# Performance work log

Hardware: AMD Instinct MI355X
Metric: run time of the kernel (lower is better)

## Reference

```python
import jax, jax.numpy as jnp
import numpy as np

D_MODEL = 1024
NUM_HEADS = 2
NUM_FEATURES = 256
DEPTH = D_MODEL // 2  # faithful to source: depth = d_model // 2
B, L = 4, 4096


def _orthogonal_gaussian(key, m, d):
    # Faithful port of orthogonal_gaussian: stacked QR blocks, scaled.
    num_squares = m // d
    remainder = m - d * num_squares
    keys = jax.random.split(key, num_squares + 1)
    blocks = []
    for i in range(num_squares):
        q, _ = jnp.linalg.qr(jax.random.normal(keys[i], (d, d)))
        blocks.append(q.T)
    if remainder:
        q, _ = jnp.linalg.qr(jax.random.normal(keys[-1], (d, d)))
        blocks.append(q.T[:remainder])
    mat = jnp.vstack(blocks)
    return mat / jnp.sqrt(jnp.float32(num_squares) + remainder / d)


def setup_inputs() -> dict:
    key = jax.random.key(0)
    ks = jax.random.split(key, 16)
    s = 0.02
    inp = {
        'query': jax.random.normal(ks[0], (B, L, D_MODEL), jnp.float32),
        'key':   jax.random.normal(ks[1], (B, L, D_MODEL), jnp.float32),
        'value': jax.random.normal(ks[2], (B, L, D_MODEL), jnp.float32),
        'mask':  jnp.zeros((B, 1, 1, L), jnp.float32),
        'Wq': jax.random.normal(ks[3], (D_MODEL, D_MODEL), jnp.float32) * s,
        'bq': jnp.zeros((D_MODEL,), jnp.float32),
        'Wk': jax.random.normal(ks[4], (D_MODEL, D_MODEL), jnp.float32) * s,
        'bk': jnp.zeros((D_MODEL,), jnp.float32),
        'Wv': jax.random.normal(ks[5], (D_MODEL, D_MODEL), jnp.float32) * s,
        'bv': jnp.zeros((D_MODEL,), jnp.float32),
        'Wo': jax.random.normal(ks[6], (D_MODEL, D_MODEL), jnp.float32) * s,
        'bo': jnp.zeros((D_MODEL,), jnp.float32),
        'random_feats': _orthogonal_gaussian(ks[7], NUM_FEATURES, DEPTH),
    }
    return inp


def _softmax_kernel(data, is_query, proj, eps=1e-6):
    # data: [B, L, H, D]; proj: [M, D]
    d = data.shape[-1]
    data = data * (1.0 / jnp.sqrt(jnp.sqrt(jnp.float32(d))))
    ratio = 1.0 / jnp.sqrt(jnp.float32(proj.shape[0]))
    data_dash = jnp.einsum('blhd,md->blhm', data, proj)  # [B,L,H,M]
    diag = jnp.sum(data * data, axis=-1, keepdims=True) * 0.5  # [B,L,H,1]
    if is_query:
        mx = jnp.max(data_dash, axis=-1, keepdims=True)
    else:
        # last_dims_t + attention_dims_t = (3, 1)
        mx = jnp.max(data_dash, axis=(3, 1), keepdims=True)
    return ratio * (jnp.exp(data_dash - diag - mx) + eps)


def _attn_hat(q, k, v, proj):
    # q,k,v: [B, H, Lh, D]  (Lh = 2L/num_heads from split_heads quirk)
    l = q.shape[0]  # faithful: tf.shape(query)[0] == batch
    q = jnp.transpose(q, (0, 2, 1, 3))  # [B, Lh, H, D]
    k = jnp.transpose(k, (0, 2, 1, 3))
    q_prime = _softmax_kernel(q, True, proj)   # [B, Lh, H, M]
    k_prime = _softmax_kernel(k, False, proj)
    v = jnp.transpose(v, (0, 2, 1, 3))         # [B, Lh, H, D]
    # Faithful einsums: axis0 labeled 'l' (=batch), axis1 labeled 'b' (=seq)
    av = jnp.einsum('lbhm,lbhd->bhmd', k_prime, v)
    av = jnp.einsum('lbhm,bhmd->lbhd', q_prime, av)
    norm = jnp.einsum('lbhm,l->bhm', k_prime, jnp.ones((l,), jnp.float32))
    norm = jnp.einsum('lbhm,bhm->lbh', q_prime, norm)
    av = jnp.transpose(av, (1, 0, 2, 3))       # [Lh, B, H, D]
    norm = jnp.transpose(norm, (1, 0, 2))[..., None]
    return av / norm


def reference(query, key, value, mask, Wq, bq, Wk, bk, Wv, bv, Wo, bo, random_feats):
    bsz = query.shape[0]
    q = query @ Wq + bq
    k = key @ Wk + bk
    v = value @ Wv + bv

    def split_heads(x):
        x = x.reshape(bsz, -1, NUM_HEADS, DEPTH)
        return jnp.transpose(x, (0, 2, 1, 3))

    q, k, v = split_heads(q), split_heads(k), split_heads(v)
    attn = _attn_hat(q, k, v, random_feats)        # [Lh, B, H, D]
    attn = jnp.transpose(attn, (0, 2, 1, 3))       # [Lh, H, B, D]
    concat = attn.reshape(bsz, -1, D_MODEL)
    return concat @ Wo + bo
```

## Files before the change

### kernel.cpp

```cpp
#include <hip/hip_runtime.h>
#include <cstdint>
#include <cstddef>

typedef unsigned short u16;
typedef __bf16 bf16x8 __attribute__((ext_vector_type(8)));
typedef float   f32x4 __attribute__((ext_vector_type(4)));

#define D_MODEL 1024
#define NF      256
#define DEPTH   512
#define SEQ     4096
#define ROWS    16384
#define HROWS   32768

#define QK_SCALE      0.21022410381342864f
#define HALF_SCALE2   0.022097086912079608f

__device__ __forceinline__ u16 f2bf(float f) {
  union { float f; uint32_t u; } x; x.f = f;
  uint32_t r = x.u + 0x7FFFu + ((x.u >> 16) & 1u);
  return (u16)(r >> 16);
}
__device__ __forceinline__ float bf2f(u16 u) {
  union { uint32_t u; float f; } x; x.u = ((uint32_t)u) << 16;
  return x.f;
}

__device__ __forceinline__ void gload16(const u16* g, u16* l) {
  __builtin_amdgcn_global_load_lds((const __attribute__((address_space(1))) void*)g,
                                   (__attribute__((address_space(3))) void*)l,
                                   16, 0, 0);
}


__global__ void cvt_kernel(const float4* __restrict__ s0, const float4* __restrict__ s1,
                           const float4* __restrict__ s2, ushort4* __restrict__ d0,
                           ushort4* __restrict__ d1, ushort4* __restrict__ d2) {
  const float4* s = (blockIdx.y == 0) ? s0 : (blockIdx.y == 1) ? s1 : s2;
  ushort4* d      = (blockIdx.y == 0) ? d0 : (blockIdx.y == 1) ? d1 : d2;
  int t = blockIdx.x * 512 + threadIdx.x;
  float4 a = s[t];
  float4 b = s[t + 256];
  d[t]       = make_ushort4(f2bf(a.x), f2bf(a.y), f2bf(a.z), f2bf(a.w));
  d[t + 256] = make_ushort4(f2bf(b.x), f2bf(b.y), f2bf(b.z), f2bf(b.w));
}

__global__ void transpose4_kernel(const float* __restrict__ w0, const float* __restrict__ w1,
                                  const float* __restrict__ w2, const float* __restrict__ w3,
                                  u16* __restrict__ o0, u16* __restrict__ o1,
                                  u16* __restrict__ o2, u16* __restrict__ o3) {
  __shared__ float tile[32][33];
  int z = blockIdx.z;
  const float* src = (z == 0) ? w0 : (z == 1) ? w1 : (z == 2) ? w2 : w3;
  u16* dst         = (z == 0) ? o0 : (z == 1) ? o1 : (z == 2) ? o2 : o3;
  int bx = blockIdx.x * 32, by = blockIdx.y * 32;
  int tx = threadIdx.x, ty = threadIdx.y;
#pragma unroll
  for (int r = ty; r < 32; r += 8) tile[r][tx] = src[(size_t)(by + r) * D_MODEL + bx + tx];
  __syncthreads();
#pragma unroll
  for (int r = ty; r < 32; r += 8)
    dst[(size_t)(bx + r) * D_MODEL + by + tx] = f2bf(tile[tx][r]);
}

__global__ void projcvt_kernel(const float4* __restrict__ p, ushort4* __restrict__ o) {
  int i = blockIdx.x * 256 + threadIdx.x;
  float4 a = p[i];
  o[i] = make_ushort4(f2bf(a.x * QK_SCALE), f2bf(a.y * QK_SCALE),
                      f2bf(a.z * QK_SCALE), f2bf(a.w * QK_SCALE));
}

template <bool BF16OUT>
__global__ __launch_bounds__(256) void gemm_bt_kernel(
    const u16* __restrict__ A, const u16* __restrict__ B, void* __restrict__ Cv,
    const float* __restrict__ bias, int K, int N) {
  __shared__ __align__(16) u16 As[128 * 32];
  __shared__ __align__(16) u16 Bs[128 * 32];
  const int tid  = threadIdx.x;
  const int lane = tid & 63;
  const int wave = tid >> 6;
  const int wm = wave >> 1, wn = wave & 1;
  const int quad = lane >> 4, l15 = lane & 15;
  const int bm = blockIdx.y, bn = blockIdx.x;
  const u16* Ab = A + (size_t)bm * 128 * K;
  const u16* Bb = B + (size_t)bn * 128 * K;

  const int srow = lane >> 2;
  const int scol = (lane & 3) * 8;
  const u16* Ag0 = Ab + (size_t)(wave * 32 + srow) * K + scol;
  const u16* Ag1 = Ag0 + (size_t)16 * K;
  const u16* Bg0 = Bb + (size_t)(wave * 32 + srow) * K + scol;
  const u16* Bg1 = Bg0 + (size_t)16 * K;
  u16* lA0 = As + wave * 1024;
  u16* lA1 = lA0 + 512;
  u16* lB0 = Bs + wave * 1024;
  u16* lB1 = lB0 + 512;

  f32x4 acc[4][4] = {};

  for (int k0 = 0; k0 < K; k0 += 32) {
    __syncthreads();
    gload16(Ag0 + k0, lA0);
    gload16(Ag1 + k0, lA1);
    gload16(Bg0 + k0, lB0);
    gload16(Bg1 + k0, lB1);
    __syncthreads();
    bf16x8 af[4], bfr[4];
#pragma unroll
    for (int mt = 0; mt < 4; mt++)
      af[mt] = *(const bf16x8*)&As[(wm * 64 + mt * 16 + l15) * 32 + quad * 8];
#pragma unroll
    for (int nt = 0; nt < 4; nt++)
      bfr[nt] = *(const bf16x8*)&Bs[(wn * 64 + nt * 16 + l15) * 32 + quad * 8];
#pragma unroll
    for (int mt = 0; mt < 4; mt++)
#pragma unroll
      for (int nt = 0; nt < 4; nt++)
        acc[mt][nt] = __builtin_amdgcn_mfma_f32_16x16x32_bf16(af[mt], bfr[nt], acc[mt][nt], 0, 0, 0);
  }

  const int rbase = bm * 128 + wm * 64 + quad * 4;
  const int cbase = bn * 128 + wn * 64 + l15;
#pragma unroll
  for (int nt = 0; nt < 4; nt++) {
    int col = cbase + nt * 16;
    float bvad = bias ? bias[col] : 0.0f;
#pragma unroll
    for (int mt = 0; mt < 4; mt++) {
#pragma unroll
      for (int r = 0; r < 4; r++) {
        int row = rbase + mt * 16 + r;
        float v = acc[mt][nt][r] + bvad;
        if (BF16OUT) ((u16*)Cv)[(size_t)row * N + col] = f2bf(v);
        else         ((float*)Cv)[(size_t)row * N + col] = v;
      }
    }
  }
}

__global__ void diag_kernel(const u16* __restrict__ Qb, const u16* __restrict__ Kb,
                            float* __restrict__ dq, float* __restrict__ dk) {
  const int wave = threadIdx.x >> 6, lane = threadIdx.x & 63;
  int row = blockIdx.x * 4 + wave;
  const u16* src; float* dst; int r;
  if (row < HROWS) { src = Qb; dst = dq; r = row; }
  else             { src = Kb; dst = dk; r = row - HROWS; }
  const ushort4* p = (const ushort4*)(src + (size_t)r * DEPTH);
  ushort4 u0 = p[lane * 2], u1 = p[lane * 2 + 1];
  float s = 0.f, f;
  f = bf2f(u0.x); s += f * f; f = bf2f(u0.y); s += f * f;
  f = bf2f(u0.z); s += f * f; f = bf2f(u0.w); s += f * f;
  f = bf2f(u1.x); s += f * f; f = bf2f(u1.y); s += f * f;
  f = bf2f(u1.z); s += f * f; f = bf2f(u1.w); s += f * f;
#pragma unroll
  for (int o = 32; o; o >>= 1) s += __shfl_xor(s, o);
  if (lane == 0) dst[r] = s * HALF_SCALE2;
}

__global__ void maxk_part_kernel(const float* __restrict__ kd, float* __restrict__ partials) {
  int g = blockIdx.x >> 6;
  int sb = blockIdx.x & 63;
  int b = g >> 1, h = g & 1;
  int tid = threadIdx.x;
  float mx = -3.4e38f;
  for (int j = 0; j < 64; j++) {
    int s = sb * 64 + j;
    int row = b * 8192 + s * 2 + h;
    mx = fmaxf(mx, kd[(size_t)row * NF + tid]);
  }
#pragma unroll
  for (int o = 32; o; o >>= 1) mx = fmaxf(mx, __shfl_xor(mx, o));
  __shared__ float wmax[4];
  if ((tid & 63) == 0) wmax[tid >> 6] = mx;
  __syncthreads();
  if (tid == 0)
    partials[blockIdx.x] = fmaxf(fmaxf(wmax[0], wmax[1]), fmaxf(wmax[2], wmax[3]));
}

__global__ void maxk_final_kernel(const float* __restrict__ partials, float* __restrict__ mxk) {
  float v = partials[blockIdx.x * 64 + threadIdx.x];
#pragma unroll
  for (int o = 32; o; o >>= 1) v = fmaxf(v, __shfl_xor(v, o));
  if (threadIdx.x == 0) mxk[blockIdx.x] = v;
}

__global__ __launch_bounds__(256) void attn_kernel(
    const float* __restrict__ qd, const float* __restrict__ kd,
    const float* __restrict__ diagq, const float* __restrict__ diagk,
    const float* __restrict__ mxk, const u16* __restrict__ Vb,
    u16* __restrict__ concat) {
  int s = blockIdx.x >> 1, h = blockIdx.x & 1;
  int t = threadIdx.x;
  int wave = t >> 6, lane = t & 63;
  __shared__ float qp[4][256], kp[4][256];
  __shared__ float As[4][4];
  __shared__ float wred[4][4];
  __shared__ float mqs[4];

  float qv[4], kv[4];
  int rows[4];
#pragma unroll
  for (int b = 0; b < 4; b++) {
    int r = b * 8192 + s * 2 + h;
    rows[b] = r;
    qv[b] = qd[(size_t)r * NF + t];
    kv[b] = kd[(size_t)r * NF + t];
  }
#pragma unroll
  for (int b = 0; b < 4; b++) {
    float v = qv[b];
#pragma unroll
    for (int o = 32; o; o >>= 1) v = fmaxf(v, __shfl_xor(v, o));
    if (lane == 0) wred[wave][b] = v;
  }
  __syncthreads();
  if (t < 4) mqs[t] = fmaxf(fmaxf(wred[0][t], wred[1][t]), fmaxf(wred[2][t], wred[3][t]));
  __syncthreads();
#pragma unroll
  for (int b = 0; b < 4; b++) {
    qp[b][t] = __expf(qv[b] - diagq[rows[b]] - mqs[b]) + 1e-6f;
    kp[b][t] = __expf(kv[b] - diagk[rows[b]] - mxk[b * 2 + h]) + 1e-6f;
  }
  __syncthreads();
  {
    int i = wave;
    float p0 = 0, p1 = 0, p2 = 0, p3 = 0;
    for (int m = lane; m < 256; m += 64) {
      float q = qp[i][m];
      p0 += q * kp[0][m]; p1 += q * kp[1][m];
      p2 += q * kp[2][m]; p3 += q * kp[3][m];
    }
#pragma unroll
    for (int o = 32; o; o >>= 1) {
      p0 += __shfl_xor(p0, o); p1 += __shfl_xor(p1, o);
      p2 += __shfl_xor(p2, o); p3 += __shfl_xor(p3, o);
    }
    if (lane == 0) { As[i][0] = p0; As[i][1] = p1; As[i][2] = p2; As[i][3] = p3; }
  }
  __syncthreads();
  float a00 = As[0][0], a01 = As[0][1], a02 = As[0][2], a03 = As[0][3];
  float a10 = As[1][0], a11 = As[1][1], a12 = As[1][2], a13 = As[1][3];
  float a20 = As[2][0], a21 = As[2][1], a22 = As[2][2], a23 = As[2][3];
  float a30 = As[3][0], a31 = As[3][1], a32 = As[3][2], a33 = As[3][3];
  float n0 = 1.f / (a00 + a01 + a02 + a03);
  float n1 = 1.f / (a10 + a11 + a12 + a13);
  float n2 = 1.f / (a20 + a21 + a22 + a23);
  float n3 = 1.f / (a30 + a31 + a32 + a33);
  size_t obase = (size_t)s * 4096 + (size_t)h * 2048;
#pragma unroll
  for (int dp = 0; dp < 2; dp++) {
    int d = t + dp * 256;
    float v0 = bf2f(Vb[((size_t)(0 * SEQ + s)) * D_MODEL + h * DEPTH + d]);
    float v1 = bf2f(Vb[((size_t)(1 * SEQ + s)) * D_MODEL + h * DEPTH + d]);
    float v2 = bf2f(Vb[((size_t)(2 * SEQ + s)) * D_MODEL + h * DEPTH + d]);
    float v3 = bf2f(Vb[((size_t)(3 * SEQ + s)) * D_MODEL + h * DEPTH + d]);
    concat[obase + 0 * 512 + d] = f2bf((a00 * v0 + a01 * v1 + a02 * v2 + a03 * v3) * n0);
    concat[obase + 1 * 512 + d] = f2bf((a10 * v0 + a11 * v1 + a12 * v2 + a13 * v3) * n1);
    concat[obase + 2 * 512 + d] = f2bf((a20 * v0 + a21 * v1 + a22 * v2 + a23 * v3) * n2);
    concat[obase + 3 * 512 + d] = f2bf((a30 * v0 + a31 * v1 + a32 * v2 + a33 * v3) * n3);
  }
}

extern "C" void kernel_launch(void* const* d_in, const int* in_sizes, int n_in,
                              void* d_out, int out_size, void* d_ws, size_t ws_size,
                              hipStream_t stream) {
  (void)in_sizes; (void)n_in; (void)out_size; (void)ws_size;
  const float* query = (const float*)d_in[0];
  const float* key   = (const float*)d_in[1];
  const float* value = (const float*)d_in[2];
  const float* Wq = (const float*)d_in[4];
  const float* bq = (const float*)d_in[5];
  const float* Wk = (const float*)d_in[6];
  const float* bk = (const float*)d_in[7];
  const float* Wv = (const float*)d_in[8];
  const float* bv = (const float*)d_in[9];
  const float* Wo = (const float*)d_in[10];
  const float* bo = (const float*)d_in[11];
  const float* proj = (const float*)d_in[12];
  float* out = (float*)d_out;

  char* w = (char*)d_ws;
  size_t o = 0;
  auto take = [&](size_t b) { void* p = w + o; o += (b + 255) & ~(size_t)255; return p; };
  u16* Xq    = (u16*)take(33554432);
  u16* Xk    = (u16*)take(33554432);
  u16* Xv    = (u16*)take(33554432);
  u16* Wqt   = (u16*)take(2097152);
  u16* Wkt   = (u16*)take(2097152);
  u16* Wvt   = (u16*)take(2097152);
  u16* Wot   = (u16*)take(2097152);
  u16* projb = (u16*)take(262144);
  u16* Qb    = (u16*)take(33554432);
  u16* Kb    = (u16*)take(33554432);
  u16* Vb    = (u16*)take(33554432);
  float* diagq    = (float*)take(131072);
  float* diagk    = (float*)take(131072);
  float* partials = (float*)take(2048);
  float* mxk      = (float*)take(64);
  float* qd   = (float*)Xq;
  float* kd   = (float*)Xk;
  u16*  concat = (u16*)Xv;

  cvt_kernel<<<dim3(8192, 3), 256, 0, stream>>>(
      (const float4*)query, (const float4*)key, (const float4*)value,
      (ushort4*)Xq, (ushort4*)Xk, (ushort4*)Xv);
  transpose4_kernel<<<dim3(32, 32, 4), dim3(32, 8), 0, stream>>>(Wq, Wk, Wv, Wo,
                                                                 Wqt, Wkt, Wvt, Wot);
  projcvt_kernel<<<128, 256, 0, stream>>>((const float4*)proj, (ushort4*)projb);

  gemm_bt_kernel<true><<<dim3(8, 128), 256, 0, stream>>>(Xq, Wqt, Qb, bq, 1024, 1024);
  gemm_bt_kernel<true><<<dim3(8, 128), 256, 0, stream>>>(Xk, Wkt, Kb, bk, 1024, 1024);
  gemm_bt_kernel<true><<<dim3(8, 128), 256, 0, stream>>>(Xv, Wvt, Vb, bv, 1024, 1024);

  diag_kernel<<<16384, 256, 0, stream>>>(Qb, Kb, diagq, diagk);

  gemm_bt_kernel<false><<<dim3(2, 256), 256, 0, stream>>>(Qb, projb, qd, nullptr, 512, 256);
  gemm_bt_kernel<false><<<dim3(2, 256), 256, 0, stream>>>(Kb, projb, kd, nullptr, 512, 256);

  maxk_part_kernel<<<512, 256, 0, stream>>>(kd, partials);
  maxk_final_kernel<<<8, 64, 0, stream>>>(partials, mxk);

  attn_kernel<<<8192, 256, 0, stream>>>(qd, kd, diagq, diagk, mxk, Vb, concat);

  gemm_bt_kernel<false><<<dim3(8, 128), 256, 0, stream>>>(concat, Wot, out, bo, 1024, 1024);
}
```

Baseline: 607.1 us.

## Fuse fp32-to-bf16 input conversion into QKV projection GEMM A-tile loads

Removes the standalone conversion kernel that turned query/key/value into bf16 buffers. The QKV GEMMs now read fp32 activations directly, convert them to bf16 in registers and write them to LDS, while B still uses direct global-to-LDS loads. The grid is also reordered so blockIdx.x walks M tiles, which changes which blocks run together and share B tiles in cache. This saves a full write and reread of three bf16 copies, at the cost of twice the global bytes per A load inside the GEMM and synchronous register staging instead of async LDS loads.

```diff
diff --git a/kernel.cpp b/kernel.cpp
--- a/kernel.cpp
+++ b/kernel.cpp
@@ -4,6 +4,7 @@
 
 typedef unsigned short u16;
 typedef __bf16 bf16x8 __attribute__((ext_vector_type(8)));
+typedef unsigned short u16x8 __attribute__((ext_vector_type(8)));
 typedef float   f32x4 __attribute__((ext_vector_type(4)));
 
 #define D_MODEL 1024
@@ -32,18 +33,6 @@
                                    16, 0, 0);
 }
 
-
-__global__ void cvt_kernel(const float4* __restrict__ s0, const float4* __restrict__ s1,
-                           const float4* __restrict__ s2, ushort4* __restrict__ d0,
-                           ushort4* __restrict__ d1, ushort4* __restrict__ d2) {
-  const float4* s = (blockIdx.y == 0) ? s0 : (blockIdx.y == 1) ? s1 : s2;
-  ushort4* d      = (blockIdx.y == 0) ? d0 : (blockIdx.y == 1) ? d1 : d2;
-  int t = blockIdx.x * 512 + threadIdx.x;
-  float4 a = s[t];
-  float4 b = s[t + 256];
-  d[t]       = make_ushort4(f2bf(a.x), f2bf(a.y), f2bf(a.z), f2bf(a.w));
-  d[t + 256] = make_ushort4(f2bf(b.x), f2bf(b.y), f2bf(b.z), f2bf(b.w));
-}
 
 __global__ void transpose4_kernel(const float* __restrict__ w0, const float* __restrict__ w1,
                                   const float* __restrict__ w2, const float* __restrict__ w3,
@@ -70,9 +59,9 @@
                       f2bf(a.z * QK_SCALE), f2bf(a.w * QK_SCALE));
 }
 
-template <bool BF16OUT>
+template <bool BF16OUT, bool AFP32>
 __global__ __launch_bounds__(256) void gemm_bt_kernel(
-    const u16* __restrict__ A, const u16* __restrict__ B, void* __restrict__ Cv,
+    const void* __restrict__ Av, const u16* __restrict__ B, void* __restrict__ Cv,
     const float* __restrict__ bias, int K, int N) {
   __shared__ __align__(16) u16 As[128 * 32];
   __shared__ __align__(16) u16 Bs[128 * 32];
@@ -81,14 +70,11 @@
   const int wave = tid >> 6;
   const int wm = wave >> 1, wn = wave & 1;
   const int quad = lane >> 4, l15 = lane & 15;
-  const int bm = blockIdx.y, bn = blockIdx.x;
-  const u16* Ab = A + (size_t)bm * 128 * K;
-  const u16* Bb = B + (size_t)bn * 128 * K;
+  const int bm = blockIdx.x, bn = blockIdx.y;
+  const u16* Bb = (const u16*)B + (size_t)bn * 128 * K;
 
   const int srow = lane >> 2;
   const int scol = (lane & 3) * 8;
-  const u16* Ag0 = Ab + (size_t)(wave * 32 + srow) * K + scol;
-  const u16* Ag1 = Ag0 + (size_t)16 * K;
   const u16* Bg0 = Bb + (size_t)(wave * 32 + srow) * K + scol;
   const u16* Bg1 = Bg0 + (size_t)16 * K;
   u16* lA0 = As + wave * 1024;
@@ -96,14 +82,44 @@
   u16* lB0 = Bs + wave * 1024;
   u16* lB1 = lB0 + 512;
 
+  const u16*   Ag0  = nullptr; const u16*   Ag1  = nullptr;
+  const float* Af0  = nullptr; const float* Af1  = nullptr;
+  if (AFP32) {
+    const float* Ab = (const float*)Av + (size_t)bm * 128 * K;
+    Af0 = Ab + (size_t)(wave * 32 + srow) * K + scol;
+    Af1 = Af0 + (size_t)16 * K;
+  } else {
+    const u16* Ab = (const u16*)Av + (size_t)bm * 128 * K;
+    Ag0 = Ab + (size_t)(wave * 32 + srow) * K + scol;
+    Ag1 = Ag0 + (size_t)16 * K;
+  }
+  u16* wA0 = As + wave * 1024 + lane * 8;
+  u16* wA1 = wA0 + 512;
+
   f32x4 acc[4][4] = {};
 
   for (int k0 = 0; k0 < K; k0 += 32) {
     __syncthreads();
-    gload16(Ag0 + k0, lA0);
-    gload16(Ag1 + k0, lA1);
-    gload16(Bg0 + k0, lB0);
-    gload16(Bg1 + k0, lB1);
+    if (AFP32) {
+      float4 p00 = *(const float4*)(Af0 + k0);
+      float4 p01 = *(const float4*)(Af0 + k0 + 4);
+      float4 p10 = *(const float4*)(Af1 + k0);
+      float4 p11 = *(const float4*)(Af1 + k0 + 4);
+      gload16(Bg0 + k0, lB0);
+      gload16(Bg1 + k0, lB1);
+      u16x8 c0, c1;
+      c0[0]=f2bf(p00.x); c0[1]=f2bf(p00.y); c0[2]=f2bf(p00.z); c0[3]=f2bf(p00.w);
+      c0[4]=f2bf(p01.x); c0[5]=f2bf(p01.y); c0[6]=f2bf(p01.z); c0[7]=f2bf(p01.w);
+      c1[0]=f2bf(p10.x); c1[1]=f2bf(p10.y); c1[2]=f2bf(p10.z); c1[3]=f2bf(p10.w);
+      c1[4]=f2bf(p11.x); c1[5]=f2bf(p11.y); c1[6]=f2bf(p11.z); c1[7]=f2bf(p11.w);
+      *(u16x8*)wA0 = c0;
+      *(u16x8*)wA1 = c1;
+    } else {
+      gload16(Ag0 + k0, lA0);
+      gload16(Ag1 + k0, lA1);
+      gload16(Bg0 + k0, lB0);
+      gload16(Bg1 + k0, lB1);
+    }
     __syncthreads();
     bf16x8 af[4], bfr[4];
 #pragma unroll
@@ -282,9 +298,6 @@
   char* w = (char*)d_ws;
   size_t o = 0;
   auto take = [&](size_t b) { void* p = w + o; o += (b + 255) & ~(size_t)255; return p; };
-  u16* Xq    = (u16*)take(33554432);
-  u16* Xk    = (u16*)take(33554432);
-  u16* Xv    = (u16*)take(33554432);
   u16* Wqt   = (u16*)take(2097152);
   u16* Wkt   = (u16*)take(2097152);
   u16* Wvt   = (u16*)take(2097152);
@@ -293,34 +306,31 @@
   u16* Qb    = (u16*)take(33554432);
   u16* Kb    = (u16*)take(33554432);
   u16* Vb    = (u16*)take(33554432);
+  float* qd  = (float*)take(33554432);
+  float* kd  = (float*)take(33554432);
+  u16* concat = (u16*)take(33554432);
   float* diagq    = (float*)take(131072);
   float* diagk    = (float*)take(131072);
   float* partials = (float*)take(2048);
   float* mxk      = (float*)take(64);
-  float* qd   = (float*)Xq;
-  float* kd   = (float*)Xk;
-  u16*  concat = (u16*)Xv;
-
-  cvt_kernel<<<dim3(8192, 3), 256, 0, stream>>>(
-      (const float4*)query, (const float4*)key, (const float4*)value,
-      (ushort4*)Xq, (ushort4*)Xk, (ushort4*)Xv);
+
   transpose4_kernel<<<dim3(32, 32, 4), dim3(32, 8), 0, stream>>>(Wq, Wk, Wv, Wo,
                                                                  Wqt, Wkt, Wvt, Wot);
   projcvt_kernel<<<128, 256, 0, stream>>>((const float4*)proj, (ushort4*)projb);
 
-  gemm_bt_kernel<true><<<dim3(8, 128), 256, 0, stream>>>(Xq, Wqt, Qb, bq, 1024, 1024);
-  gemm_bt_kernel<true><<<dim3(8, 128), 256, 0, stream>>>(Xk, Wkt, Kb, bk, 1024, 1024);
-  gemm_bt_kernel<true><<<dim3(8, 128), 256, 0, stream>>>(Xv, Wvt, Vb, bv, 1024, 1024);
+  gemm_bt_kernel<true, true><<<dim3(128, 8), 256, 0, stream>>>(query, Wqt, Qb, bq, 1024, 1024);
+  gemm_bt_kernel<true, true><<<dim3(128, 8), 256, 0, stream>>>(key,   Wkt, Kb, bk, 1024, 1024);
+  gemm_bt_kernel<true, true><<<dim3(128, 8), 256, 0, stream>>>(value, Wvt, Vb, bv, 1024, 1024);
 
   diag_kernel<<<16384, 256, 0, stream>>>(Qb, Kb, diagq, diagk);
 
-  gemm_bt_kernel<false><<<dim3(2, 256), 256, 0, stream>>>(Qb, projb, qd, nullptr, 512, 256);
-  gemm_bt_kernel<false><<<dim3(2, 256), 256, 0, stream>>>(Kb, projb, kd, nullptr, 512, 256);
+  gemm_bt_kernel<false, false><<<dim3(256, 2), 256, 0, stream>>>(Qb, projb, qd, nullptr, 512, 256);
+  gemm_bt_kernel<false, false><<<dim3(256, 2), 256, 0, stream>>>(Kb, projb, kd, nullptr, 512, 256);
 
   maxk_part_kernel<<<512, 256, 0, stream>>>(kd, partials);
   maxk_final_kernel<<<8, 64, 0, stream>>>(partials, mxk);
 
   attn_kernel<<<8192, 256, 0, stream>>>(qd, kd, diagq, diagk, mxk, Vb, concat);
 
-  gemm_bt_kernel<false><<<dim3(8, 128), 256, 0, stream>>>(concat, Wot, out, bo, 1024, 1024);
-}
+  gemm_bt_kernel<false, false><<<dim3(128, 8), 256, 0, stream>>>(concat, Wot, out, bo, 1024, 1024);
+}
```

Result: slower. 621.2 us (+2.3%).
